# Kernel tuning notes

Measured on AMD Instinct MI355X. Metric: run time of the kernel, lower is better.

## Reference

```python
import jax, jax.numpy as jnp
import numpy as np
from itertools import product as _prod

N_CODONS = 16
S = 6 * N_CODONS + 12          # 108 states
N_EMIT = 126                    # (4+1)**3 + 1 transformed emission ids
CODE = {'A': [0], 'C': [1], 'G': [2], 'T': [3], 'N': [0, 1, 2, 3], 'X': [5]}


def _emission_structure(n):
    """Static (state, kmer_id, weight_index) triples; widx=-1 means constant 1."""
    calls = [(0, 'N', 0, True), (1, 'A', 0, True), (2, 'AT', 0, True),
             (3, 'ATG', 2, False), (4, 'ATGN', 2, True), (5, 'ATGNN', 2, True)]
    for s in range(6, 6 + 3 * n - 2):
        calls.append((s, 'N', 2, True))
    calls += [(4 + 3 * n, 'T', 2, True), (5 + 3 * n, 'TA', 2, True), (5 + 3 * n, 'TG', 2, True),
              (6 + 3 * n, 'TAA', 2, False), (6 + 3 * n, 'TAG', 2, False), (6 + 3 * n, 'TGA', 2, False),
              (7 + 3 * n, 'N', 2, True)]
    for s in range(8 + 3 * n, 8 + 3 * n + 3 * (n + 1)):
        calls.append((s, 'N', 2, True))
    term1 = 8 + 3 * n + 3 * (n + 1)
    calls.append((term1, 'X', 2, True))
    rows, cols, widx = [], [], []
    k = 0
    for state, em, xmust, trainable in calls:
        if em[-1] == 'X':
            rows.append(state); cols.append(125); widx.append(-1)
            continue
        prefix = ['N'] * max(0, 2 - len(em) + 1)
        syms = (prefix + list(em))[-3:]
        allowed = [CODE[e] + ([4] if i < 2 - xmust else []) for i, e in enumerate(syms)]
        for x in _prod(*allowed):
            found, ok = False, True
            for i in range(2):
                if found and x[i] == 4:
                    ok = False
                    break
                if x[i] != 4:
                    found = True
            if not ok:
                continue
            rows.append(state); cols.append(x[0] * 25 + x[1] * 5 + x[2])
            widx.append(k if trainable else -1)
            if trainable:
                k += 1
    return np.array(rows), np.array(cols), np.array(widx)

E_ROWS, E_COLS, E_WIDX = _emission_structure(N_CODONS)


def _sparse_row_softmax(vals, rows, cols, shape):
    m = jax.ops.segment_max(vals, rows, num_segments=shape[0])
    e = jnp.exp(vals - m[rows])
    z = jax.ops.segment_sum(e, rows, num_segments=shape[0])
    return jnp.zeros(shape, vals.dtype).at[rows, cols].set(e / z[rows])


def _build_A(w, n):
    off, term1 = 8 + 3 * n, 11 + 6 * n
    rows = [0, 0, 1, 2]; cols = [0, 1, 2, 3]
    pieces = [jnp.stack([1.0 - w[0], w[0]]), jnp.ones(2, w.dtype)]
    k = 1
    rows += [3 + 3 * i for i in range(n)]; cols += [4 + 3 * i for i in range(n)]
    pieces.append(w[k:k + n]); k += n
    rows += [4 + 3 * i for i in range(n)]; cols += [5 + 3 * i for i in range(n)]
    rows += [5 + 3 * i for i in range(n)]; cols += [6 + 3 * i for i in range(n)]
    pieces.append(jnp.ones(2 * n, w.dtype))
    rows += [3 + 3 * i for i in range(n + 1)]; cols += [off + 3 * i for i in range(n + 1)]
    pieces.append(w[k:k + n + 1]); k += n + 1
    rows += [3 + 3 * n]; cols += [4 + 3 * n]
    pieces.append(w[k:k + 1]); k += 1
    rows += [off + 3 * i for i in range(n + 1)]; cols += [off + 1 + 3 * i for i in range(n + 1)]
    rows += [off + 1 + 3 * i for i in range(n + 1)]; cols += [off + 2 + 3 * i for i in range(n + 1)]
    pieces.append(jnp.ones(2 * (n + 1), w.dtype))
    rows += [off + 2 + 3 * i for i in range(n + 1)]; cols += [4 + 3 * i for i in range(n + 1)]
    pieces.append(w[k:k + n + 1])
    rows += [off + 2 + 3 * i for i in range(n + 1)]; cols += [off + 3 * i for i in range(n + 1)]
    pieces.append(1.0 - w[k:k + n + 1]); k += n + 1
    i_del = [3 + 3 * i for i in range(n) for _ in range(n - i)]
    j_del = [4 + 3 * j for i in range(1, n + 1) for j in range(i, n + 1)]
    rows += i_del; cols += j_del
    exps = np.array([(jj - ii) // 3 + 1 for ii, jj in zip(i_del, j_del)], np.float32)
    wk = w[k]; k += 1
    sgn = jnp.where(np.mod(exps, 2) == 1, jnp.sign(wk), 1.0)  # (-w)**int exp without nan
    pieces.append(1.0 - sgn * jnp.abs(wk) ** exps)
    rows += [4 + 3 * n, 5 + 3 * n, 6 + 3 * n, 7 + 3 * n, 7 + 3 * n, term1]
    cols += [5 + 3 * n, 6 + 3 * n, 7 + 3 * n, 7 + 3 * n, term1, term1]
    pieces.append(jnp.ones(6, w.dtype))
    vals = jnp.concatenate(pieces)
    return _sparse_row_softmax(vals, np.array(rows), np.array(cols), (S, S))


def _build_B(ek):
    vals = jnp.where(E_WIDX >= 0, ek[np.maximum(E_WIDX, 0)], 1.0)
    return _sparse_row_softmax(vals, E_ROWS, E_COLS, (S, N_EMIT))


def setup_inputs() -> dict:
    key = jax.random.key(0)
    k1, k2, k3, k4 = jax.random.split(key, 4)
    # pure k-mer ids (base-5 digits in 0..3) so every symbol is emittable
    d = jax.random.randint(k1, (256, 2048, 3), 0, 4)
    inputs = (d[..., 0] * 25 + d[..., 1] * 5 + d[..., 2]).astype(jnp.int32)
    return {
        'inputs': inputs,
        'transition_kernel': 0.05 * jax.random.normal(k2, (3 * N_CODONS + 5,), jnp.float32),
        'emission_kernel': 0.05 * jax.random.normal(k3, (S * 216,), jnp.float32),
        'init_kernel': 0.05 * jax.random.normal(k4, (S,), jnp.float32),
    }


def reference(inputs, transition_kernel, emission_kernel, init_kernel):
    A = _build_A(transition_kernel, N_CODONS)      # [S, S] sparse-softmaxed transitions
    Bt = _build_B(emission_kernel).T               # [N_EMIT, S] emission probs
    pi = jax.nn.softmax(init_kernel)
    a0 = pi[None, :] * Bt[inputs[:, 0]]            # [batch, S]
    a0 = a0 / a0.sum(-1, keepdims=True)

    def step(alpha, e_t):
        a = (alpha @ A) * Bt[e_t]                  # sparse matvec + emission gather
        a = a / a.sum(-1, keepdims=True)           # per-step normalization
        return a, a

    _, ys = jax.lax.scan(step, a0, inputs[:, 1:].T)
    alphas = jnp.concatenate([a0[None], ys], axis=0)  # [T, batch, S]
    return jnp.transpose(alphas, (1, 0, 2))           # [batch, T, S]
```

## Files before the change

kernel.cpp:

```cpp
#include <hip/hip_runtime.h>
#include <cstdint>
#include <cstddef>

#define S 108
#define NEMIT 126
#define T_LEN 2048
#define N_BATCH 256
#define MAXG 10
#define MAXNE 6500
#define NE_A 280
#define TRASH_IDX (32 * S)

#define RESCALE_TARGET 1e24f

struct EmTab {
  short row[MAXNE];
  short col[MAXNE];
  short widx[MAXNE];
  int rp[S + 1];
  int n;
  int nw;
};

constexpr int cmask(int sym, int add4) {
  int m = (sym == 4) ? 0xF : (1 << sym);
  if (add4) m |= 0x10;
  return m;
}

constexpr EmTab buildEm() {
  EmTab E{};
  int n = 0, k = 0;
  auto doCall = [&](int stt, int s0_, int s1_, int s2_, int xm_, int tr_) {
    const int m0 = cmask(s0_, xm_ < 2 ? 1 : 0);
    const int m1 = cmask(s1_, xm_ < 1 ? 1 : 0);
    const int m2 = cmask(s2_, 0);
    for (int x0 = 0; x0 < 5; x0++) {
      if (!((m0 >> x0) & 1)) continue;
      for (int x1 = 0; x1 < 5; x1++) {
        if (!((m1 >> x1) & 1)) continue;
        if (x0 != 4 && x1 == 4) continue;
        for (int x2 = 0; x2 < 5; x2++) {
          if (!((m2 >> x2) & 1)) continue;
          E.row[n] = (short)stt;
          E.col[n] = (short)(x0 * 25 + x1 * 5 + x2);
          E.widx[n] = (short)(tr_ ? k++ : -1);
          n++;
        }
      }
    }
  };
  doCall(0, 4, 4, 4, 0, 1);
  doCall(1, 4, 4, 0, 0, 1);
  doCall(2, 4, 0, 3, 0, 1);
  doCall(3, 0, 3, 2, 2, 0);
  doCall(4, 3, 2, 4, 2, 1);
  doCall(5, 2, 4, 4, 2, 1);
  for (int s = 6; s <= 51; s++) doCall(s, 4, 4, 4, 2, 1);
  doCall(52, 4, 4, 3, 2, 1);
  doCall(53, 4, 3, 0, 2, 1);
  doCall(53, 4, 3, 2, 2, 1);
  doCall(54, 3, 0, 0, 2, 0);
  doCall(54, 3, 0, 2, 2, 0);
  doCall(54, 3, 2, 0, 2, 0);
  doCall(55, 4, 4, 4, 2, 1);
  for (int s = 56; s <= 106; s++) doCall(s, 4, 4, 4, 2, 1);
  E.row[n] = 107; E.col[n] = 125; E.widx[n] = -1; n++;
  E.n = n; E.nw = k;
  for (int r = 0; r <= S; r++) E.rp[r] = 0;
  for (int e = 0; e < n; e++) E.rp[E.row[e] + 1]++;
  for (int r = 0; r < S; r++) E.rp[r + 1] += E.rp[r];
  return E;
}

constexpr EmTab EM_HOST = buildEm();
static_assert(EM_HOST.n <= MAXNE && EM_HOST.n > 6000, "emission count sanity");
__device__ const EmTab g_em = EM_HOST;

struct APlan {
  short vcode[NE_A], vwi[NE_A];
  short aidx[NE_A];
  short arp[S + 1];
  unsigned char src[64][MAXG];
  short a0[64][MAXG], a1[64][MAXG];
  unsigned char d0[64], d1[64], b0[64], b1[64];
  short o0[64], o1[64], scol[64];
  unsigned char sm1[64], sm2[64];
  int maxload, ncons, np;
};

constexpr APlan buildPlan() {
  APlan P{};
  short arow[NE_A] = {}, acol[NE_A] = {};
  int ne = 0;
  auto AD = [&](int r, int c, int code, int wi) {
    arow[ne] = (short)r; acol[ne] = (short)c;
    P.vcode[ne] = (short)code; P.vwi[ne] = (short)wi; ne++;
  };
  AD(0, 0, 2, 0); AD(0, 1, 1, 0); AD(1, 2, 0, 0); AD(2, 3, 0, 0);
  for (int i = 0; i < 16; i++) AD(3 + 3 * i, 4 + 3 * i, 1, 1 + i);
  for (int i = 0; i < 16; i++) AD(4 + 3 * i, 5 + 3 * i, 0, 0);
  for (int i = 0; i < 16; i++) AD(5 + 3 * i, 6 + 3 * i, 0, 0);
  for (int i = 0; i <= 16; i++) AD(3 + 3 * i, 56 + 3 * i, 1, 17 + i);
  AD(51, 52, 1, 34);
  for (int i = 0; i <= 16; i++) AD(56 + 3 * i, 57 + 3 * i, 0, 0);
  for (int i = 0; i <= 16; i++) AD(57 + 3 * i, 58 + 3 * i, 0, 0);
  for (int i = 0; i <= 16; i++) AD(58 + 3 * i, 4 + 3 * i, 1, 35 + i);
  for (int i = 0; i <= 16; i++) AD(58 + 3 * i, 56 + 3 * i, 2, 35 + i);
  for (int a = 0; a < 16; a++)
    for (int jj = a + 1; jj <= 16; jj++) AD(3 + 3 * a, 4 + 3 * jj, 3, jj - a + 1);
  AD(52, 53, 0, 0); AD(53, 54, 0, 0); AD(54, 55, 0, 0);
  AD(55, 55, 0, 0); AD(55, 107, 0, 0); AD(107, 107, 0, 0);

  int rc[S + 1] = {};
  for (int e = 0; e < ne; e++) rc[arow[e] + 1]++;
  for (int r = 0; r < S; r++) rc[r + 1] += rc[r];
  for (int r = 0; r <= S; r++) P.arp[r] = (short)rc[r];
  int fill[S] = {};
  for (int e = 0; e < ne; e++) { const int r = arow[e]; P.aidx[rc[r] + fill[r]] = (short)e; fill[r]++; }

  int ccnt[S] = {}; short clist[S][18] = {};
  for (int e = 0; e < ne; e++) { const int c = acol[e]; clist[c][ccnt[c]] = (short)e; ccnt[c]++; }
  int npcA[S] = {};
  short pdefs[16][6] = {}; int pcnt[16] = {}; short pcol[16] = {};
  int np = 0;
  for (int c = 0; c < S; c++) {
    while (ccnt[c] > 8) {
      const int base = ccnt[c] - 6;
      for (int j = 0; j < 6; j++) pdefs[np][j] = clist[c][base + j];
      pcnt[np] = 6; pcol[np] = (short)c;
      npcA[c]++; ccnt[c] -= 6; np++;
    }
  }
  int lload[64] = {}, lnit[64] = {};
  for (int l = 0; l < 64; l++) {
    for (int e = 0; e < MAXG; e++) { P.src[l][e] = 0; P.a0[l][e] = -1; P.a1[l][e] = -1; }
    P.d0[l] = 127; P.d1[l] = 127; P.b0[l] = 0; P.b1[l] = 0;
    P.o0[l] = -1; P.o1[l] = -1; P.scol[l] = -1; P.sm1[l] = 0; P.sm2[l] = 0;
  }
  int ncons = 0;
  for (int c = 0; c < S; c++) {
    if (ccnt[c] == 1) {
      const int e0 = clist[c][0];
      const int r = arow[e0];
      if (npcA[r] > 0) {
        const int l = 54 + ncons; ncons++;
        int k = 0;
        P.src[l][k] = (unsigned char)r; P.a0[l][k] = (short)e0; k++;
        for (int p = 0; p < np; p++)
          if (pcol[p] == r) { P.src[l][k] = (unsigned char)(108 + p); P.a0[l][k] = (short)e0; k++; }
        P.d0[l] = (unsigned char)c; P.b0[l] = (unsigned char)c; P.o0[l] = (short)c;
        P.scol[l] = (short)r;
        P.sm1[l] = (k >= 2) ? 1 : 0; P.sm2[l] = (k >= 3) ? 1 : 0;
        lload[l] = k; lnit[l] = 1;
        ccnt[c] = 0;
      }
    }
  }
  int rr = 0;
  auto pickLane = [&](int L) {
    for (;;) {
      const int pos = rr & 127; rr++;
      const int l = (pos < 64) ? pos : (127 - pos);
      if (lnit[l] < 2 && lload[l] + L <= MAXG) return l;
    }
  };
  for (int th = 8; th >= 1; th--) {
    for (int p = 0; p < np; p++) {
      if (pcnt[p] != th) continue;
      const int l = pickLane(th);
      const int it = lnit[l], base = lload[l];
      for (int j = 0; j < th; j++) {
        P.src[l][base + j] = (unsigned char)arow[pdefs[p][j]];
        if (it == 0) P.a0[l][base + j] = pdefs[p][j];
        else         P.a1[l][base + j] = pdefs[p][j];
      }
      if (it == 0) { P.d0[l] = (unsigned char)(108 + p); P.b0[l] = (unsigned char)pcol[p]; P.o0[l] = -1; }
      else         { P.d1[l] = (unsigned char)(108 + p); P.b1[l] = (unsigned char)pcol[p]; P.o1[l] = -1; }
      lload[l] = base + th; lnit[l] = it + 1;
    }
    for (int c = 0; c < S; c++) {
      if (ccnt[c] != th) continue;
      const int l = pickLane(th);
      const int it = lnit[l], base = lload[l];
      for (int j = 0; j < th; j++) {
        P.src[l][base + j] = (unsigned char)arow[clist[c][j]];
        if (it == 0) P.a0[l][base + j] = clist[c][j];
        else         P.a1[l][base + j] = clist[c][j];
      }
      const short oc = (npcA[c] > 0) ? (short)-1 : (short)c;
      if (it == 0) { P.d0[l] = (unsigned char)c; P.b0[l] = (unsigned char)c; P.o0[l] = oc; }
      else         { P.d1[l] = (unsigned char)c; P.b1[l] = (unsigned char)c; P.o1[l] = oc; }
      lload[l] = base + th; lnit[l] = it + 1;
    }
  }
  int ml = 0;
  for (int l = 0; l < 64; l++) ml = (lload[l] > ml) ? lload[l] : ml;
  P.maxload = ml; P.ncons = ncons; P.np = np;
  return P;
}

constexpr APlan PLAN_HOST = buildPlan();
static_assert(PLAN_HOST.maxload <= MAXG, "lane gather overflow");
static_assert(PLAN_HOST.ncons <= 10, "too many consumer lanes");
static_assert(PLAN_HOST.np <= 16, "too many pieces");
__device__ const APlan g_plan = PLAN_HOST;

#define PSTEP(SYM_, RS_, PRS_, RESC_, SCOK_)                              \
  {                                                                       \
    const int ecur_ = (SYM_);                                             \
    float x[MAXG];                                                        \
    _Pragma("unroll")                                                     \
    for (int e = 0; e < MAXG; e++) x[e] = alpha_lds[gsrc[e]];             \
    const float bt0_ = Bt_lds[ecur_ * S + b0c];                           \
    const float bt1_ = Bt_lds[ecur_ * S + b1c];                           \
    float aA_ = 0.f, aB_ = 0.f, bA_ = 0.f, bB_ = 0.f;                     \
    _Pragma("unroll")                                                     \
    for (int e = 0; e < MAXG; e += 2) {                                   \
      aA_ += x[e] * w0v[e];     aB_ += x[e + 1] * w0v[e + 1];             \
      bA_ += x[e] * w1v[e];     bB_ += x[e + 1] * w1v[e + 1];             \
    }                                                                     \
    u0 = (aA_ + aB_) * bt0_;                                              \
    u1 = (bA_ + bB_) * bt1_;                                              \
    const float sumv_ = x[0] + sm1 * x[1] + sm2 * x[2];                   \
    if (RESC_) {                                                          \
      float m_ = fmaxf(u0, u1);                                           \
      _Pragma("unroll")                                                   \
      for (int msk_ = 1; msk_ < 64; msk_ <<= 1)                           \
        m_ = fmaxf(m_, __shfl_xor(m_, msk_, 64));                         \
      const float r_ = RESCALE_TARGET / m_;                               \
      u0 *= r_; u1 *= r_;                                                 \
    }                                                                     \
    alpha_lds[d0] = u0;                                                   \
    alpha_lds[d1] = u1;                                                   \
    const int a0_ = (o0 >= 0) ? (RS_) + o0 : TRASH_IDX;                   \
    const int a1_ = (o1 >= 0) ? (RS_) + o1 : TRASH_IDX;                   \
    ring[a0_] = u0;                                                       \
    ring[a1_] = u1;                                                       \
    if (SCOK_) {                                                          \
      const int a2_ = (scol >= 0) ? (PRS_) + scol : TRASH_IDX;            \
      ring[a2_] = sumv_;                                                  \
    }                                                                     \
  }

__global__ __launch_bounds__(128, 1) void hmm_scan_kernel(
    const int* __restrict__ inp, const float* __restrict__ w,
    const float* __restrict__ ek, const float* __restrict__ ik,
    float* __restrict__ out) {
  __shared__ __align__(16) float Bt_lds[NEMIT * S];
  __shared__ __align__(16) float ring[32 * S + 4];
  __shared__ float alpha_lds[128];
  __shared__ float pi_lds[S];
  __shared__ float avalS[NE_A];
  __shared__ __align__(16) int seq_lds[T_LEN + 16];

  const int tid = threadIdx.x;
  const int lid = tid & 63;
  const int wv = tid >> 6;

  for (int i = tid; i < NEMIT * S; i += 128) Bt_lds[i] = 0.f;

  {
    const int4* s4 = (const int4*)(inp + (size_t)blockIdx.x * T_LEN);
    int4* d4 = (int4*)seq_lds;
    for (int i = tid; i < T_LEN / 4; i += 128) d4[i] = s4[i];
    if (tid < 4) d4[T_LEN / 4 + tid] = s4[T_LEN / 4 - 1];
  }

  if (wv == 0) {
    float q0 = ik[lid];
    float q1 = (lid + 64 < S) ? ik[lid + 64] : -1e30f;
    float mx = fmaxf(q0, q1);
#pragma unroll
    for (int msk = 1; msk < 64; msk <<= 1) mx = fmaxf(mx, __shfl_xor(mx, msk, 64));
    float e0v = expf(q0 - mx);
    float e1v = (lid + 64 < S) ? expf(q1 - mx) : 0.f;
    float zz = e0v + e1v;
#pragma unroll
    for (int msk = 1; msk < 64; msk <<= 1) zz += __shfl_xor(zz, msk, 64);
    const float rz = 1.f / zz;
    pi_lds[lid] = e0v * rz;
    if (lid + 64 < S) pi_lds[lid + 64] = e1v * rz;
  }

  {
    const float wk = w[52];
    const float aw = fabsf(wk);
    const float sgnw = (wk > 0.f) ? 1.f : ((wk < 0.f) ? -1.f : 0.f);
    for (int e = tid; e < NE_A; e += 128) {
      const int code = g_plan.vcode[e];
      const int wi = g_plan.vwi[e];
      float v;
      if (code == 0) v = 1.f;
      else if (code == 1) v = w[wi];
      else if (code == 2) v = 1.f - w[wi];
      else {
        const float pw = powf(aw, (float)wi);
        v = 1.f - ((wi & 1) ? sgnw : 1.f) * pw;
      }
      avalS[e] = v;
    }
  }
  __syncthreads();

  if (tid < S) {
    const int b = g_plan.arp[tid], e2 = g_plan.arp[tid + 1];
    float m = -1e30f;
    for (int j = b; j < e2; j++) m = fmaxf(m, avalS[g_plan.aidx[j]]);
    float z = 0.f;
    for (int j = b; j < e2; j++) z += expf(avalS[g_plan.aidx[j]] - m);
    const float rz = 1.f / z;
    for (int j = b; j < e2; j++) {
      const int ii = g_plan.aidx[j];
      avalS[ii] = expf(avalS[ii] - m) * rz;
    }
  }
  __syncthreads();

  if (tid < S) {
    const int r = tid;
    const int b = g_em.rp[r], e2 = g_em.rp[r + 1];
    float m = -1e30f;
    for (int e = b; e < e2; e++) {
      const int wi = g_em.widx[e];
      m = fmaxf(m, (wi >= 0) ? ek[wi] : 1.f);
    }
    float z = 0.f;
    for (int e = b; e < e2; e++) {
      const int wi = g_em.widx[e];
      z += expf(((wi >= 0) ? ek[wi] : 1.f) - m);
    }
    const float rz = 1.f / z;
    for (int e = b; e < e2; e++) {
      const int wi = g_em.widx[e];
      Bt_lds[(int)g_em.col[e] * S + r] = expf(((wi >= 0) ? ek[wi] : 1.f) - m) * rz;
    }
  }

  int gsrc[MAXG]; float w0v[MAXG], w1v[MAXG];
#pragma unroll
  for (int e = 0; e < MAXG; e++) {
    gsrc[e] = g_plan.src[lid][e];
    const int a0 = g_plan.a0[lid][e], a1 = g_plan.a1[lid][e];
    w0v[e] = (a0 >= 0) ? avalS[a0] : 0.f;
    w1v[e] = (a1 >= 0) ? avalS[a1] : 0.f;
  }
  const int d0 = g_plan.d0[lid], d1 = g_plan.d1[lid];
  const int b0c = g_plan.b0[lid], b1c = g_plan.b1[lid];
  const int o0 = g_plan.o0[lid], o1 = g_plan.o1[lid];
  const int scol = g_plan.scol[lid];
  const float sm1 = (float)g_plan.sm1[lid], sm2 = (float)g_plan.sm2[lid];
  __syncthreads();

  float* ob = out + (size_t)blockIdx.x * T_LEN * S;
  int etn = 0;
  float u0 = 0.f, u1 = 0.f;

  if (wv == 0) {
    const int e0s = seq_lds[0];
    const float ui0 = (d0 < 108) ? RESCALE_TARGET * pi_lds[d0] * Bt_lds[e0s * S + d0] : 0.f;
    const float ui1 = (d1 < 108) ? RESCALE_TARGET * pi_lds[d1] * Bt_lds[e0s * S + d1] : 0.f;
    alpha_lds[d0] = ui0;
    alpha_lds[d1] = ui1;
    for (int i = lid; i < S; i += 64) ring[i] = alpha_lds[i];
    etn = seq_lds[1];
  }

  for (int k = 0; k <= 128; k++) {
    if (wv == 0) {
      if (k < 128) {
        const int tb = 16 * k;
        const int hb = (k & 1) << 4;
        int rs = hb * S;
        if (k == 0) {
          rs += S;
          for (int j = 1; j < 15; j++) {
            const int ec = etn; etn = seq_lds[j + 1];
            PSTEP(ec, rs, rs - S, 0, 1)
            rs += S;
          }
          const int ec = etn; etn = seq_lds[16];
          PSTEP(ec, rs, rs - S, 1, 1)
        } else {
          {
            const int ec = etn; etn = seq_lds[tb + 1];
            PSTEP(ec, rs, 0, 0, 0)
            rs += S;
          }
          for (int j = 1; j < 15; j++) {
            const int ec = etn; etn = seq_lds[tb + j + 1];
            PSTEP(ec, rs, rs - S, 0, 1)
            rs += S;
          }
          const int ec = etn; etn = seq_lds[tb + 16];
          PSTEP(ec, rs, rs - S, 1, 1)
        }
        if (scol >= 0) {
          const float x0 = alpha_lds[gsrc[0]];
          const float x1 = alpha_lds[gsrc[1]];
          const float x2 = alpha_lds[gsrc[2]];
          ring[(hb + 15) * S + scol] = x0 + sm1 * x1 + sm2 * x2;
        }
      }
    } else {
      if (k > 0) {
        const int g = k - 1;
        const float4* srcb4 = (const float4*)&ring[(g & 1) * 16 * S];
        float4* dstb4 = (float4*)(ob + (size_t)g * 16 * S);
        const int r = lid >> 2;
        const int j = lid & 3;
        float4 v0, v1, v2, v3, v4, v5, v6;
        float psum = 0.f;
        v6 = make_float4(0.f, 0.f, 0.f, 0.f);
        const int base4 = r * 27 + j;
        v0 = srcb4[base4];
        v1 = srcb4[base4 + 4];
        v2 = srcb4[base4 + 8];
        v3 = srcb4[base4 + 12];
        v4 = srcb4[base4 + 16];
        v5 = srcb4[base4 + 20];
        if (j < 3) v6 = srcb4[base4 + 24];
        psum = v0.x + v0.y + v0.z + v0.w + v1.x + v1.y + v1.z + v1.w
             + v2.x + v2.y + v2.z + v2.w + v3.x + v3.y + v3.z + v3.w
             + v4.x + v4.y + v4.z + v4.w + v5.x + v5.y + v5.z + v5.w
             + v6.x + v6.y + v6.z + v6.w;
        psum += __shfl_xor(psum, 1, 64);
        psum += __shfl_xor(psum, 2, 64);
        const float iv = 1.f / psum;
        v0.x *= iv; v0.y *= iv; v0.z *= iv; v0.w *= iv;
        v1.x *= iv; v1.y *= iv; v1.z *= iv; v1.w *= iv;
        v2.x *= iv; v2.y *= iv; v2.z *= iv; v2.w *= iv;
        v3.x *= iv; v3.y *= iv; v3.z *= iv; v3.w *= iv;
        v4.x *= iv; v4.y *= iv; v4.z *= iv; v4.w *= iv;
        v5.x *= iv; v5.y *= iv; v5.z *= iv; v5.w *= iv;
        v6.x *= iv; v6.y *= iv; v6.z *= iv; v6.w *= iv;
        dstb4[base4] = v0;
        dstb4[base4 + 4] = v1;
        dstb4[base4 + 8] = v2;
        dstb4[base4 + 12] = v3;
        dstb4[base4 + 16] = v4;
        dstb4[base4 + 20] = v5;
        if (j < 3) dstb4[base4 + 24] = v6;
      }
    }
    __syncthreads();
  }
}

extern "C" void kernel_launch(void* const* d_in, const int* in_sizes, int n_in,
                              void* d_out, int out_size, void* d_ws, size_t ws_size,
                              hipStream_t stream) {
  const int* inp = (const int*)d_in[0];
  const float* w = (const float*)d_in[1];
  const float* ek = (const float*)d_in[2];
  const float* ik = (const float*)d_in[3];
  float* out = (float*)d_out;
  (void)d_ws; (void)ws_size; (void)in_sizes; (void)n_in; (void)out_size;
  hmm_scan_kernel<<<N_BATCH, 128, 0, stream>>>(inp, w, ek, ik, out);
}
```

Baseline: 413.3 us.

## Gather alpha directly from padded ring rows instead of a separate alpha buffer

Removes the separate alpha_lds scratch vector. Each step now writes its results straight into a ring row padded to 132 floats, with piece slots in columns 108..121, and the next step gathers from the previous ring row. This drops the extra LDS write and the trash-index logic from the serial per-step chain. The cost is more complex indexing, including special handling of the weights for consumer lanes at the first step of each chunk, and a larger ring in LDS.

```diff
diff --git a/kernel.cpp b/kernel.cpp
--- a/kernel.cpp
+++ b/kernel.cpp
@@ -9,7 +9,7 @@
 #define MAXG 10
 #define MAXNE 6500
 #define NE_A 280
-#define TRASH_IDX (32 * S)
+#define RW 132
 
 #define RESCALE_TARGET 1e24f
 
@@ -84,7 +84,7 @@
   unsigned char src[64][MAXG];
   short a0[64][MAXG], a1[64][MAXG];
   unsigned char d0[64], d1[64], b0[64], b1[64];
-  short o0[64], o1[64], scol[64];
+  short scol[64];
   unsigned char sm1[64], sm2[64];
   int maxload, ncons, np;
 };
@@ -136,7 +136,7 @@
   for (int l = 0; l < 64; l++) {
     for (int e = 0; e < MAXG; e++) { P.src[l][e] = 0; P.a0[l][e] = -1; P.a1[l][e] = -1; }
     P.d0[l] = 127; P.d1[l] = 127; P.b0[l] = 0; P.b1[l] = 0;
-    P.o0[l] = -1; P.o1[l] = -1; P.scol[l] = -1; P.sm1[l] = 0; P.sm2[l] = 0;
+    P.scol[l] = -1; P.sm1[l] = 0; P.sm2[l] = 0;
   }
   int ncons = 0;
   for (int c = 0; c < S; c++) {
@@ -149,7 +149,7 @@
         P.src[l][k] = (unsigned char)r; P.a0[l][k] = (short)e0; k++;
         for (int p = 0; p < np; p++)
           if (pcol[p] == r) { P.src[l][k] = (unsigned char)(108 + p); P.a0[l][k] = (short)e0; k++; }
-        P.d0[l] = (unsigned char)c; P.b0[l] = (unsigned char)c; P.o0[l] = (short)c;
+        P.d0[l] = (unsigned char)c; P.b0[l] = (unsigned char)c;
         P.scol[l] = (short)r;
         P.sm1[l] = (k >= 2) ? 1 : 0; P.sm2[l] = (k >= 3) ? 1 : 0;
         lload[l] = k; lnit[l] = 1;
@@ -175,8 +175,8 @@
         if (it == 0) P.a0[l][base + j] = pdefs[p][j];
         else         P.a1[l][base + j] = pdefs[p][j];
       }
-      if (it == 0) { P.d0[l] = (unsigned char)(108 + p); P.b0[l] = (unsigned char)pcol[p]; P.o0[l] = -1; }
-      else         { P.d1[l] = (unsigned char)(108 + p); P.b1[l] = (unsigned char)pcol[p]; P.o1[l] = -1; }
+      if (it == 0) { P.d0[l] = (unsigned char)(108 + p); P.b0[l] = (unsigned char)pcol[p]; }
+      else         { P.d1[l] = (unsigned char)(108 + p); P.b1[l] = (unsigned char)pcol[p]; }
       lload[l] = base + th; lnit[l] = it + 1;
     }
     for (int c = 0; c < S; c++) {
@@ -188,9 +188,8 @@
         if (it == 0) P.a0[l][base + j] = clist[c][j];
         else         P.a1[l][base + j] = clist[c][j];
       }
-      const short oc = (npcA[c] > 0) ? (short)-1 : (short)c;
-      if (it == 0) { P.d0[l] = (unsigned char)c; P.b0[l] = (unsigned char)c; P.o0[l] = oc; }
-      else         { P.d1[l] = (unsigned char)c; P.b1[l] = (unsigned char)c; P.o1[l] = oc; }
+      if (it == 0) { P.d0[l] = (unsigned char)c; P.b0[l] = (unsigned char)c; }
+      else         { P.d1[l] = (unsigned char)c; P.b1[l] = (unsigned char)c; }
       lload[l] = base + th; lnit[l] = it + 1;
     }
   }
@@ -203,21 +202,21 @@
 constexpr APlan PLAN_HOST = buildPlan();
 static_assert(PLAN_HOST.maxload <= MAXG, "lane gather overflow");
 static_assert(PLAN_HOST.ncons <= 10, "too many consumer lanes");
-static_assert(PLAN_HOST.np <= 16, "too many pieces");
+static_assert(PLAN_HOST.np <= 14, "piece slots must fit cols 108..121");
 __device__ const APlan g_plan = PLAN_HOST;
 
-#define PSTEP(SYM_, RS_, PRS_, RESC_, SCOK_)                              \
+#define PSTEP(SYM_, RS_, GB_, RESC_, SCOK_, W0_)                          \
   {                                                                       \
     const int ecur_ = (SYM_);                                             \
     float x[MAXG];                                                        \
     _Pragma("unroll")                                                     \
-    for (int e = 0; e < MAXG; e++) x[e] = alpha_lds[gsrc[e]];             \
+    for (int e = 0; e < MAXG; e++) x[e] = ring[(GB_) + gsrc[e]];          \
     const float bt0_ = Bt_lds[ecur_ * S + b0c];                           \
     const float bt1_ = Bt_lds[ecur_ * S + b1c];                           \
     float aA_ = 0.f, aB_ = 0.f, bA_ = 0.f, bB_ = 0.f;                     \
     _Pragma("unroll")                                                     \
     for (int e = 0; e < MAXG; e += 2) {                                   \
-      aA_ += x[e] * w0v[e];     aB_ += x[e + 1] * w0v[e + 1];             \
+      aA_ += x[e] * W0_[e];     aB_ += x[e + 1] * W0_[e + 1];             \
       bA_ += x[e] * w1v[e];     bB_ += x[e + 1] * w1v[e + 1];             \
     }                                                                     \
     u0 = (aA_ + aB_) * bt0_;                                              \
@@ -231,14 +230,10 @@
       const float r_ = RESCALE_TARGET / m_;                               \
       u0 *= r_; u1 *= r_;                                                 \
     }                                                                     \
-    alpha_lds[d0] = u0;                                                   \
-    alpha_lds[d1] = u1;                                                   \
-    const int a0_ = (o0 >= 0) ? (RS_) + o0 : TRASH_IDX;                   \
-    const int a1_ = (o1 >= 0) ? (RS_) + o1 : TRASH_IDX;                   \
-    ring[a0_] = u0;                                                       \
-    ring[a1_] = u1;                                                       \
+    ring[(RS_) + d0] = u0;                                                \
+    ring[(RS_) + d1] = u1;                                                \
     if (SCOK_) {                                                          \
-      const int a2_ = (scol >= 0) ? (PRS_) + scol : TRASH_IDX;            \
+      const int a2_ = (scol >= 0) ? (GB_) + scol : (GB_) + 123 + (lid & 3); \
       ring[a2_] = sumv_;                                                  \
     }                                                                     \
   }
@@ -248,8 +243,7 @@
     const float* __restrict__ ek, const float* __restrict__ ik,
     float* __restrict__ out) {
   __shared__ __align__(16) float Bt_lds[NEMIT * S];
-  __shared__ __align__(16) float ring[32 * S + 4];
-  __shared__ float alpha_lds[128];
+  __shared__ __align__(16) float ring[32 * RW];
   __shared__ float pi_lds[S];
   __shared__ float avalS[NE_A];
   __shared__ __align__(16) int seq_lds[T_LEN + 16];
@@ -347,9 +341,13 @@
   }
   const int d0 = g_plan.d0[lid], d1 = g_plan.d1[lid];
   const int b0c = g_plan.b0[lid], b1c = g_plan.b1[lid];
-  const int o0 = g_plan.o0[lid], o1 = g_plan.o1[lid];
   const int scol = g_plan.scol[lid];
   const float sm1 = (float)g_plan.sm1[lid], sm2 = (float)g_plan.sm2[lid];
+
+  float w0j[MAXG];
+#pragma unroll
+  for (int e = 0; e < MAXG; e++) w0j[e] = w0v[e];
+  if (scol >= 0) { w0j[1] = 0.f; w0j[2] = 0.f; }
   __syncthreads();
 
   float* ob = out + (size_t)blockIdx.x * T_LEN * S;
@@ -360,9 +358,8 @@
     const int e0s = seq_lds[0];
     const float ui0 = (d0 < 108) ? RESCALE_TARGET * pi_lds[d0] * Bt_lds[e0s * S + d0] : 0.f;
     const float ui1 = (d1 < 108) ? RESCALE_TARGET * pi_lds[d1] * Bt_lds[e0s * S + d1] : 0.f;
-    alpha_lds[d0] = ui0;
-    alpha_lds[d1] = ui1;
-    for (int i = lid; i < S; i += 64) ring[i] = alpha_lds[i];
+    ring[d0] = ui0;
+    ring[d1] = ui1;
     etn = seq_lds[1];
   }
 
@@ -371,59 +368,61 @@
       if (k < 128) {
         const int tb = 16 * k;
         const int hb = (k & 1) << 4;
-        int rs = hb * S;
+        int rs = hb * RW;
         if (k == 0) {
-          rs += S;
+          rs += RW;
           for (int j = 1; j < 15; j++) {
             const int ec = etn; etn = seq_lds[j + 1];
-            PSTEP(ec, rs, rs - S, 0, 1)
-            rs += S;
+            PSTEP(ec, rs, rs - RW, 0, 1, w0v)
+            rs += RW;
           }
           const int ec = etn; etn = seq_lds[16];
-          PSTEP(ec, rs, rs - S, 1, 1)
+          PSTEP(ec, rs, rs - RW, 1, 1, w0v)
         } else {
+          const int gb0 = (((k & 1) ^ 1) * 16 + 15) * RW;
           {
             const int ec = etn; etn = seq_lds[tb + 1];
-            PSTEP(ec, rs, 0, 0, 0)
-            rs += S;
+            PSTEP(ec, rs, gb0, 0, 0, w0j)
+            rs += RW;
           }
           for (int j = 1; j < 15; j++) {
             const int ec = etn; etn = seq_lds[tb + j + 1];
-            PSTEP(ec, rs, rs - S, 0, 1)
-            rs += S;
+            PSTEP(ec, rs, rs - RW, 0, 1, w0v)
+            rs += RW;
           }
           const int ec = etn; etn = seq_lds[tb + 16];
-          PSTEP(ec, rs, rs - S, 1, 1)
+          PSTEP(ec, rs, rs - RW, 1, 1, w0v)
         }
         if (scol >= 0) {
-          const float x0 = alpha_lds[gsrc[0]];
-          const float x1 = alpha_lds[gsrc[1]];
-          const float x2 = alpha_lds[gsrc[2]];
-          ring[(hb + 15) * S + scol] = x0 + sm1 * x1 + sm2 * x2;
+          const int base = (hb + 15) * RW;
+          const float x0 = ring[base + gsrc[0]];
+          const float x1 = ring[base + gsrc[1]];
+          const float x2 = ring[base + gsrc[2]];
+          ring[base + scol] = x0 + sm1 * x1 + sm2 * x2;
         }
       }
     } else {
       if (k > 0) {
         const int g = k - 1;
-        const float4* srcb4 = (const float4*)&ring[(g & 1) * 16 * S];
+        const float4* srcb4 = (const float4*)&ring[(g & 1) * 16 * RW];
         float4* dstb4 = (float4*)(ob + (size_t)g * 16 * S);
         const int r = lid >> 2;
         const int j = lid & 3;
         float4 v0, v1, v2, v3, v4, v5, v6;
-        float psum = 0.f;
         v6 = make_float4(0.f, 0.f, 0.f, 0.f);
-        const int base4 = r * 27 + j;
-        v0 = srcb4[base4];
-        v1 = srcb4[base4 + 4];
-        v2 = srcb4[base4 + 8];
-        v3 = srcb4[base4 + 12];
-        v4 = srcb4[base4 + 16];
-        v5 = srcb4[base4 + 20];
-        if (j < 3) v6 = srcb4[base4 + 24];
-        psum = v0.x + v0.y + v0.z + v0.w + v1.x + v1.y + v1.z + v1.w
-             + v2.x + v2.y + v2.z + v2.w + v3.x + v3.y + v3.z + v3.w
-             + v4.x + v4.y + v4.z + v4.w + v5.x + v5.y + v5.z + v5.w
-             + v6.x + v6.y + v6.z + v6.w;
+        const int sbase = r * 33 + j;
+        const int dbase = r * 27 + j;
+        v0 = srcb4[sbase];
+        v1 = srcb4[sbase + 4];
+        v2 = srcb4[sbase + 8];
+        v3 = srcb4[sbase + 12];
+        v4 = srcb4[sbase + 16];
+        v5 = srcb4[sbase + 20];
+        if (j < 3) v6 = srcb4[sbase + 24];
+        float psum = v0.x + v0.y + v0.z + v0.w + v1.x + v1.y + v1.z + v1.w
+                   + v2.x + v2.y + v2.z + v2.w + v3.x + v3.y + v3.z + v3.w
+                   + v4.x + v4.y + v4.z + v4.w + v5.x + v5.y + v5.z + v5.w
+                   + v6.x + v6.y + v6.z + v6.w;
         psum += __shfl_xor(psum, 1, 64);
         psum += __shfl_xor(psum, 2, 64);
         const float iv = 1.f / psum;
@@ -434,13 +433,13 @@
         v4.x *= iv; v4.y *= iv; v4.z *= iv; v4.w *= iv;
         v5.x *= iv; v5.y *= iv; v5.z *= iv; v5.w *= iv;
         v6.x *= iv; v6.y *= iv; v6.z *= iv; v6.w *= iv;
-        dstb4[base4] = v0;
-        dstb4[base4 + 4] = v1;
-        dstb4[base4 + 8] = v2;
-        dstb4[base4 + 12] = v3;
-        dstb4[base4 + 16] = v4;
-        dstb4[base4 + 20] = v5;
-        if (j < 3) dstb4[base4 + 24] = v6;
+        dstb4[dbase] = v0;
+        dstb4[dbase + 4] = v1;
+        dstb4[dbase + 8] = v2;
+        dstb4[dbase + 12] = v3;
+        dstb4[dbase + 16] = v4;
+        dstb4[dbase + 20] = v5;
+        if (j < 3) dstb4[dbase + 24] = v6;
       }
     }
     __syncthreads();
```

New measurement: 375.5 us. 9.2% less time.
